# Kernel tuning notes

Measured on AMD Instinct MI355X. Metric: run time of the kernel, lower is better.

Reference implementation:

```python
import jax, jax.numpy as jnp
import numpy as np

N = 4096      # tokens per modality
DIM = 514     # input feature dim
OUT = 256     # out_dim (per-head width, head=1)
NC = 2        # num_classes
LN_EPS = 1e-5


def setup_inputs() -> dict:
    key = jax.random.key(0)
    ks = jax.random.split(key, 12)
    def nrm(k, shape, s=0.02):
        return jax.random.normal(k, shape, dtype=jnp.float32) * s
    return {
        "t1": jax.random.normal(ks[0], (N, DIM), dtype=jnp.float32),
        "t2": jax.random.normal(ks[1], (N, DIM), dtype=jnp.float32),
        "t1c": jax.random.normal(ks[2], (N, DIM), dtype=jnp.float32),
        "Wqkv1": nrm(ks[3], (DIM, 3 * OUT)), "bqkv1": jnp.zeros((3 * OUT,), jnp.float32),
        "Wqkv2": nrm(ks[4], (DIM, 3 * OUT)), "bqkv2": jnp.zeros((3 * OUT,), jnp.float32),
        "Wqkv3": nrm(ks[5], (DIM, 3 * OUT)), "bqkv3": jnp.zeros((3 * OUT,), jnp.float32),
        "Wo1": nrm(ks[6], (2 * OUT, DIM)), "bo1": jnp.zeros((DIM,), jnp.float32),
        "Wo2": nrm(ks[7], (2 * OUT, DIM)), "bo2": jnp.zeros((DIM,), jnp.float32),
        "Wo3": nrm(ks[8], (2 * OUT, DIM)), "bo3": jnp.zeros((DIM,), jnp.float32),
        "ln_g": jnp.ones((3 * DIM,), jnp.float32),
        "ln_b": jnp.zeros((3 * DIM,), jnp.float32),
        "Wh": nrm(ks[9], (3 * DIM, NC)), "bh": jnp.zeros((NC,), jnp.float32),
    }


def _forward(t1, t2, t1c, Wqkv1, bqkv1, Wqkv2, bqkv2, Wqkv3, bqkv3,
             Wo1, bo1, Wo2, bo2, Wo3, bo3, ln_g, ln_b, Wh, bh):
    # QKV projections (head=1 so no head reshape needed)
    q1, k1, v1 = jnp.split(t1 @ Wqkv1 + bqkv1, 3, axis=-1)   # each [n, OUT]
    q2, k2, v2 = jnp.split(t2 @ Wqkv2 + bqkv2, 3, axis=-1)
    q3, k3, v3 = jnp.split(t1c @ Wqkv3 + bqkv3, 3, axis=-1)

    # Six cross-attention instances batched into one group dim g=6.
    # Order: out12, out13, out21, out23, out31, out32  (q_x attends to k_y/v_y)
    qs = jnp.stack([q2, q3, q1, q3, q1, q2])                  # [6, n, OUT]
    ks_ = jnp.stack([k1, k1, k2, k2, k3, k3])
    vs = jnp.stack([v1, v1, v2, v2, v3, v3])
    # NOTE: original code applies NO 1/sqrt(d) scale
    attn = jax.nn.softmax(jnp.einsum('gid,gjd->gij', qs, ks_), axis=-1)
    outs = jnp.einsum('gij,gjd->gid', attn, vs)               # [6, n, OUT]
    out12, out13, out21, out23, out31, out32 = outs

    # residual add with duplicated keys, then per-modality output proj + residual
    t1r = jnp.concatenate([out21, out31], -1) + jnp.concatenate([k1, k1], -1)
    t2r = jnp.concatenate([out12, out32], -1) + jnp.concatenate([k2, k2], -1)
    t3r = jnp.concatenate([out13, out23], -1) + jnp.concatenate([k3, k3], -1)
    a1 = t1r @ Wo1 + bo1 + t1                                 # [n, DIM]
    a2 = t2r @ Wo2 + bo2 + t2
    a3 = t3r @ Wo3 + bo3 + t1c

    atten = jnp.concatenate([a1, a2, a3], -1)                 # [n, 3*DIM]
    mu = jnp.mean(atten, axis=-1, keepdims=True)
    var = jnp.var(atten, axis=-1, keepdims=True)
    normed = (atten - mu) * jax.lax.rsqrt(var + LN_EPS) * ln_g + ln_b
    out = normed @ Wh + bh                                    # [n, NC]
    feat = atten[None]                                        # [1, n, 3*DIM]
    return out, feat


def reference(t1, t2, t1c, Wqkv1, bqkv1, Wqkv2, bqkv2, Wqkv3, bqkv3,
              Wo1, bo1, Wo2, bo2, Wo3, bo3, ln_g, ln_b, Wh, bh):
    return _forward(t1, t2, t1c, Wqkv1, bqkv1, Wqkv2, bqkv2, Wqkv3, bqkv3,
                    Wo1, bo1, Wo2, bo2, Wo3, bo3, ln_g, ln_b, Wh, bh)
```

## Files before the change

### kernel.cpp

```cpp
#include <hip/hip_runtime.h>
#include <hip/hip_bf16.h>

typedef unsigned short u16;
typedef unsigned int u32;
typedef __attribute__((ext_vector_type(8))) __bf16 bf16x8;
typedef __attribute__((ext_vector_type(16))) float f32x16;

#define N_TOK 4096
#define DIMF  514
#define KPAD  544
#define OUT3  768
#define OUTD  256
#define RDIM  512
#define FDIM  1542
#define SHIFT 16.0f
#define NCHUNK 4
#define KTILES ((N_TOK / NCHUNK) / 32)

__device__ __forceinline__ bf16x8 ld_frag(const u16* p) {
    return __builtin_bit_cast(bf16x8, *reinterpret_cast<const uint4*>(p));
}
__device__ __forceinline__ u16 f2bf(float x) {
    return __builtin_bit_cast(u16, __float2bfloat16(x));
}
__device__ __forceinline__ float bf2f(u16 u) {
    return __bfloat162float(__builtin_bit_cast(__hip_bfloat16, u));
}
__device__ __forceinline__ f32x16 mfma_b(bf16x8 a, bf16x8 b, f32x16 c) {
    return __builtin_amdgcn_mfma_f32_32x32x16_bf16(a, b, c, 0, 0, 0);
}
__device__ __forceinline__ void gl_lds16(const u16* g, u16* l) {
    __builtin_amdgcn_global_load_lds(
        (const __attribute__((address_space(1))) void*)(g),
        (__attribute__((address_space(3))) void*)(l), 16, 0, 0);
}

__global__ void prep_kernel(const float* __restrict__ t1, const float* __restrict__ t2,
                            const float* __restrict__ t1c,
                            const float* __restrict__ W1, const float* __restrict__ W2,
                            const float* __restrict__ W3,
                            const float* __restrict__ Wo1, const float* __restrict__ Wo2,
                            const float* __restrict__ Wo3,
                            u16* __restrict__ tA, u16* __restrict__ WqkvT,
                            u16* __restrict__ WoT)
{
    int idx = blockIdx.x * blockDim.x + threadIdx.x;
    const int TA_N = 3 * N_TOK * KPAD;
    const int WQ_N = 3 * OUT3 * KPAD;
    const int WO_N = 3 * DIMF * RDIM;
    if (idx < TA_N) {
        int m = idx / (N_TOK * KPAD);
        int rem = idx - m * (N_TOK * KPAD);
        int row = rem / KPAD;
        int col = rem - row * KPAD;
        const float* t = (m == 0) ? t1 : (m == 1) ? t2 : t1c;
        tA[idx] = (col < DIMF) ? f2bf(t[row * DIMF + col]) : (u16)0;
    } else if (idx < TA_N + WQ_N) {
        int i = idx - TA_N;
        int m = i / (OUT3 * KPAD);
        int rem = i - m * (OUT3 * KPAD);
        int n = rem / KPAD;
        int c = rem - n * KPAD;
        const float* W = (m == 0) ? W1 : (m == 1) ? W2 : W3;
        WqkvT[i] = (c < DIMF) ? f2bf(W[c * OUT3 + n]) : (u16)0;
    } else if (idx < TA_N + WQ_N + WO_N) {
        int i = idx - TA_N - WQ_N;
        int m = i / (DIMF * RDIM);
        int rem = i - m * (DIMF * RDIM);
        int n = rem / RDIM;
        int c = rem - n * RDIM;
        const float* W = (m == 0) ? Wo1 : (m == 1) ? Wo2 : Wo3;
        WoT[i] = f2bf(W[c * DIMF + n]);
    }
}

__global__ __launch_bounds__(256, 1) void qkv_gemm(
    const u16* __restrict__ tA, const u16* __restrict__ WqkvT,
    const float* __restrict__ b1, const float* __restrict__ b2, const float* __restrict__ b3,
    u16* __restrict__ qbuf, u16* __restrict__ kbuf, u16* __restrict__ vT)
{
    const int mt = blockIdx.x, nt = blockIdx.y, mod = blockIdx.z;
    const u16* A = tA + mod * (N_TOK * KPAD);
    const u16* B = WqkvT + mod * (OUT3 * KPAD);
    const float* bias = (mod == 0) ? b1 : (mod == 1) ? b2 : b3;

    __shared__ alignas(16) u16 Al[128 * 40];
    __shared__ alignas(16) u16 Bl[128 * 40];

    const int tid = threadIdx.x;
    const int lane = tid & 63;
    const int w = tid >> 6;
    const int wm = w & 1, wn = w >> 1;
    const int l31 = lane & 31, h = lane >> 5;

    f32x16 acc[2][2];
#pragma unroll
    for (int i = 0; i < 2; i++)
#pragma unroll
        for (int j = 0; j < 2; j++)
#pragma unroll
            for (int r = 0; r < 16; r++) acc[i][j][r] = 0.f;

    for (int kt = 0; kt < KPAD / 32; kt++) {
#pragma unroll
        for (int it = 0; it < 2; it++) {
            int idx = it * 256 + tid;
            int row = idx >> 2;
            int c8 = (idx & 3) * 8;
            uint4 va = *reinterpret_cast<const uint4*>(&A[(mt * 128 + row) * KPAD + kt * 32 + c8]);
            *reinterpret_cast<uint4*>(&Al[row * 40 + c8]) = va;
            uint4 vb = *reinterpret_cast<const uint4*>(&B[(nt * 128 + row) * KPAD + kt * 32 + c8]);
            *reinterpret_cast<uint4*>(&Bl[row * 40 + c8]) = vb;
        }
        __syncthreads();
#pragma unroll
        for (int kc = 0; kc < 2; kc++) {
            bf16x8 af[2], bfr[2];
#pragma unroll
            for (int mr = 0; mr < 2; mr++)
                af[mr] = ld_frag(&Al[(wm * 64 + mr * 32 + l31) * 40 + kc * 16 + h * 8]);
#pragma unroll
            for (int nr = 0; nr < 2; nr++)
                bfr[nr] = ld_frag(&Bl[(wn * 64 + nr * 32 + l31) * 40 + kc * 16 + h * 8]);
#pragma unroll
            for (int mr = 0; mr < 2; mr++)
#pragma unroll
                for (int nr = 0; nr < 2; nr++)
                    acc[mr][nr] = mfma_b(af[mr], bfr[nr], acc[mr][nr]);
        }
        __syncthreads();
    }

    u16* qb = qbuf + mod * (N_TOK * OUTD);
    u16* kb = kbuf + mod * (N_TOK * OUTD);
    u16* vb = vT + mod * (OUTD * N_TOK);
#pragma unroll
    for (int mr = 0; mr < 2; mr++)
#pragma unroll
        for (int nr = 0; nr < 2; nr++)
#pragma unroll
            for (int r = 0; r < 16; r++) {
                int row = mt * 128 + wm * 64 + mr * 32 + (r & 3) + 8 * (r >> 2) + 4 * h;
                int col = nt * 128 + wn * 64 + nr * 32 + l31;
                u16 bv = f2bf(acc[mr][nr][r] + bias[col]);
                int cs = col >> 8, cc = col & 255;
                if (cs == 0)      qb[row * OUTD + cc] = bv;
                else if (cs == 1) kb[row * OUTD + cc] = bv;
                else              vb[cc * N_TOK + row] = bv;
            }
}

__global__ __launch_bounds__(256, 2) void attn_kernel(
    const u16* __restrict__ qbuf, const u16* __restrict__ kbuf,
    const u16* __restrict__ vT, u16* __restrict__ Opart, float* __restrict__ lpart)
{
    const int qt = blockIdx.x;
    const int g  = blockIdx.y;
    const int c  = blockIdx.z;
    const int kv = g >> 1;
    const int mn = (kv == 0) ? 1 : 0;
    const int mx = (kv == 2) ? 1 : 2;
    const int qm = (g & 1) ? mx : mn;

    const u16* Qg = qbuf + qm * (N_TOK * OUTD);
    const u16* Kg = kbuf + kv * (N_TOK * OUTD);
    const u16* Vg = vT + kv * (OUTD * N_TOK);
    u16* Op = Opart + ((size_t)(c * 6 + g) * N_TOK + qt * 128) * OUTD;
    float* lp = lpart + (c * 6 + g) * N_TOK + qt * 128;

    __shared__ alignas(16) u16 Fbuf[2][32 * 512];

    const int tid = threadIdx.x;
    const int lane = tid & 63;
    const int w = tid >> 6;
    const int l31 = lane & 31, h = lane >> 5;
    const int q0 = qt * 128 + w * 32;

    auto stage = [&](int k0, u16* dst) {
        if (w < 2) {
#pragma unroll
            for (int fi = 0; fi < 8; fi++) {
                int dc = w * 8 + fi;
                gl_lds16(&Kg[(k0 + l31) * OUTD + dc * 16 + h * 8], dst + dc * 512);
            }
        } else {
#pragma unroll
            for (int fi = 0; fi < 8; fi++) {
                int f = (w - 2) * 8 + fi;
                int nb = f >> 1, half = f & 1;
                gl_lds16(&Vg[(nb * 32 + l31) * N_TOK + k0 + half * 16 + h * 8],
                         dst + (16 + f) * 512);
            }
        }
    };

    const int k0base = c * (N_TOK / NCHUNK);

    stage(k0base, Fbuf[0]);

    bf16x8 qf[16];
#pragma unroll
    for (int dc = 0; dc < 16; dc++)
        qf[dc] = ld_frag(&Qg[(q0 + l31) * OUTD + dc * 16 + h * 8]);

    f32x16 Oacc[8];
#pragma unroll
    for (int nb = 0; nb < 8; nb++)
#pragma unroll
        for (int r = 0; r < 16; r++) Oacc[nb][r] = 0.f;
    float lsum = 0.f;

    __syncthreads();

    for (int kt = 0; kt < KTILES; kt++) {
        const int p = kt & 1;
        if (kt + 1 < KTILES) stage(k0base + (kt + 1) * 32, Fbuf[p ^ 1]);
        const u16* FB = Fbuf[p];

        f32x16 S;
#pragma unroll
        for (int r = 0; r < 16; r++) S[r] = 0.f;
#pragma unroll
        for (int dc = 0; dc < 16; dc++) {
            bf16x8 kf = ld_frag(&FB[dc * 512 + lane * 8]);
            S = mfma_b(kf, qf[dc], S);
        }

        float e[16];
#pragma unroll
        for (int r = 0; r < 16; r++) { e[r] = __expf(S[r] - SHIFT); lsum += e[r]; }
        u32 pk[8];
#pragma unroll
        for (int i = 0; i < 8; i++)
            pk[i] = (u32)f2bf(e[2 * i]) | ((u32)f2bf(e[2 * i + 1]) << 16);
        u32 x[8];
#pragma unroll
        for (int i = 0; i < 8; i++)
            x[i] = (u32)__shfl_xor((int)pk[i], 32, 64);
        uint4 b0, b1;
        b0.x = h ? x[2] : pk[0]; b0.y = h ? x[3] : pk[1];
        b0.z = h ? pk[2] : x[0]; b0.w = h ? pk[3] : x[1];
        b1.x = h ? x[6] : pk[4]; b1.y = h ? x[7] : pk[5];
        b1.z = h ? pk[6] : x[4]; b1.w = h ? pk[7] : x[5];
        bf16x8 pb0 = __builtin_bit_cast(bf16x8, b0);
        bf16x8 pb1 = __builtin_bit_cast(bf16x8, b1);

#pragma unroll
        for (int nb = 0; nb < 8; nb++) {
            bf16x8 vf0 = ld_frag(&FB[(16 + 2 * nb) * 512 + lane * 8]);
            bf16x8 vf1 = ld_frag(&FB[(17 + 2 * nb) * 512 + lane * 8]);
            Oacc[nb] = mfma_b(vf0, pb0, Oacc[nb]);
            Oacc[nb] = mfma_b(vf1, pb1, Oacc[nb]);
        }
        __syncthreads();
    }

    lsum += __shfl_xor(lsum, 32, 64);
    if (lane < 32) lp[w * 32 + lane] = lsum;

    float* Tb = reinterpret_cast<float*>(&Fbuf[0][0]) + w * (32 * 33);
#pragma unroll
    for (int nb = 0; nb < 8; nb++) {
#pragma unroll
        for (int r = 0; r < 16; r++)
            Tb[((r & 3) + 8 * (r >> 2) + 4 * h) * 33 + l31] = Oacc[nb][r];
        __builtin_amdgcn_s_waitcnt(0);
#pragma unroll
        for (int qq = 0; qq < 16; qq++) {
            float v = Tb[l31 * 33 + qq * 2 + h];
            Op[(w * 32 + qq * 2 + h) * OUTD + nb * 32 + l31] = f2bf(v);
        }
        __builtin_amdgcn_s_waitcnt(0);
    }
}

__global__ __launch_bounds__(256, 1) void combine_kernel(
    const u16* __restrict__ Opart, const float* __restrict__ lpart,
    const u16* __restrict__ kbuf, u16* __restrict__ rbuf)
{
    const int q = blockIdx.x;
    const int g = blockIdx.y;
    const int d = threadIdx.x;
    const int kv = g >> 1;
    const int mn = (kv == 0) ? 1 : 0;
    const int mx = (kv == 2) ? 1 : 2;
    const int qm = (g & 1) ? mx : mn;
    const int sm = (qm == 0) ? 1 : 0;
    const int slot = (kv == sm) ? 0 : 1;

    float o = 0.f, l = 0.f;
#pragma unroll
    for (int c = 0; c < NCHUNK; c++) {
        o += bf2f(Opart[((size_t)(c * 6 + g) * N_TOK + q) * OUTD + d]);
        l += lpart[(c * 6 + g) * N_TOK + q];
    }
    float res = o / l + bf2f(kbuf[qm * (N_TOK * OUTD) + q * OUTD + d]);
    rbuf[qm * (size_t)(N_TOK * RDIM) + q * RDIM + slot * OUTD + d] = f2bf(res);
}

__global__ __launch_bounds__(256, 1) void proj_gemm(
    const u16* __restrict__ rbuf, const u16* __restrict__ WoT,
    const float* __restrict__ bo1, const float* __restrict__ bo2, const float* __restrict__ bo3,
    const float* __restrict__ t1, const float* __restrict__ t2, const float* __restrict__ t1c,
    float* __restrict__ feat)
{
    const int mt = blockIdx.x, nt = blockIdx.y, mod = blockIdx.z;
    const u16* A = rbuf + mod * (N_TOK * RDIM);
    const u16* B = WoT + mod * (DIMF * RDIM);
    const float* bias = (mod == 0) ? bo1 : (mod == 1) ? bo2 : bo3;
    const float* tres = (mod == 0) ? t1 : (mod == 1) ? t2 : t1c;

    __shared__ alignas(16) u16 Al[128 * 40];
    __shared__ alignas(16) u16 Bl[128 * 40];

    const int tid = threadIdx.x;
    const int lane = tid & 63;
    const int w = tid >> 6;
    const int wm = w & 1, wn = w >> 1;
    const int l31 = lane & 31, h = lane >> 5;

    f32x16 acc[2][2];
#pragma unroll
    for (int i = 0; i < 2; i++)
#pragma unroll
        for (int j = 0; j < 2; j++)
#pragma unroll
            for (int r = 0; r < 16; r++) acc[i][j][r] = 0.f;

    for (int kt = 0; kt < RDIM / 32; kt++) {
#pragma unroll
        for (int it = 0; it < 2; it++) {
            int idx = it * 256 + tid;
            int row = idx >> 2;
            int c8 = (idx & 3) * 8;
            uint4 va = *reinterpret_cast<const uint4*>(&A[(mt * 128 + row) * RDIM + kt * 32 + c8]);
            *reinterpret_cast<uint4*>(&Al[row * 40 + c8]) = va;
            int n = nt * 128 + row;
            uint4 vb;
            if (n < DIMF) vb = *reinterpret_cast<const uint4*>(&B[n * RDIM + kt * 32 + c8]);
            else { vb.x = vb.y = vb.z = vb.w = 0u; }
            *reinterpret_cast<uint4*>(&Bl[row * 40 + c8]) = vb;
        }
        __syncthreads();
#pragma unroll
        for (int kc = 0; kc < 2; kc++) {
            bf16x8 af[2], bfr[2];
#pragma unroll
            for (int mr = 0; mr < 2; mr++)
                af[mr] = ld_frag(&Al[(wm * 64 + mr * 32 + l31) * 40 + kc * 16 + h * 8]);
#pragma unroll
            for (int nr = 0; nr < 2; nr++)
                bfr[nr] = ld_frag(&Bl[(wn * 64 + nr * 32 + l31) * 40 + kc * 16 + h * 8]);
#pragma unroll
            for (int mr = 0; mr < 2; mr++)
#pragma unroll
                for (int nr = 0; nr < 2; nr++)
                    acc[mr][nr] = mfma_b(af[mr], bfr[nr], acc[mr][nr]);
        }
        __syncthreads();
    }

#pragma unroll
    for (int mr = 0; mr < 2; mr++)
#pragma unroll
        for (int nr = 0; nr < 2; nr++)
#pragma unroll
            for (int r = 0; r < 16; r++) {
                int row = mt * 128 + wm * 64 + mr * 32 + (r & 3) + 8 * (r >> 2) + 4 * h;
                int col = nt * 128 + wn * 64 + nr * 32 + l31;
                if (col < DIMF) {
                    float v = acc[mr][nr][r] + bias[col] + tres[row * DIMF + col];
                    feat[row * FDIM + mod * DIMF + col] = v;
                }
            }
}

__global__ __launch_bounds__(256, 1) void ln_head(
    const float* __restrict__ feat, const float* __restrict__ gam,
    const float* __restrict__ bet, const float* __restrict__ Wh,
    const float* __restrict__ bh, float* __restrict__ out)
{
    const int row = blockIdx.x;
    const float* x = feat + row * FDIM;
    const int tid = threadIdx.x;
    float v[7];
    float s = 0.f, ss = 0.f;
#pragma unroll
    for (int i = 0; i < 7; i++) {
        int idx = tid + i * 256;
        float val = (idx < FDIM) ? x[idx] : 0.f;
        v[i] = val; s += val; ss += val * val;
    }
#pragma unroll
    for (int m = 1; m < 64; m <<= 1) { s += __shfl_xor(s, m, 64); ss += __shfl_xor(ss, m, 64); }
    __shared__ float red[8];
    const int w = tid >> 6, lane = tid & 63;
    if (lane == 0) { red[w] = s; red[4 + w] = ss; }
    __syncthreads();
    s = red[0] + red[1] + red[2] + red[3];
    ss = red[4] + red[5] + red[6] + red[7];
    const float mu = s / (float)FDIM;
    const float var = ss / (float)FDIM - mu * mu;
    const float rstd = rsqrtf(var + 1e-5f);
    float a0 = 0.f, a1 = 0.f;
#pragma unroll
    for (int i = 0; i < 7; i++) {
        int idx = tid + i * 256;
        if (idx < FDIM) {
            float nv = (v[i] - mu) * rstd * gam[idx] + bet[idx];
            a0 += nv * Wh[idx * 2];
            a1 += nv * Wh[idx * 2 + 1];
        }
    }
#pragma unroll
    for (int m = 1; m < 64; m <<= 1) { a0 += __shfl_xor(a0, m, 64); a1 += __shfl_xor(a1, m, 64); }
    __shared__ float red2[8];
    if (lane == 0) { red2[w] = a0; red2[4 + w] = a1; }
    __syncthreads();
    if (tid == 0) {
        out[row * 2 + 0] = red2[0] + red2[1] + red2[2] + red2[3] + bh[0];
        out[row * 2 + 1] = red2[4] + red2[5] + red2[6] + red2[7] + bh[1];
    }
}

extern "C" void kernel_launch(void* const* d_in, const int* in_sizes, int n_in,
                              void* d_out, int out_size, void* d_ws, size_t ws_size,
                              hipStream_t stream)
{
    const float* t1    = (const float*)d_in[0];
    const float* t2    = (const float*)d_in[1];
    const float* t1c   = (const float*)d_in[2];
    const float* Wqkv1 = (const float*)d_in[3];
    const float* bqkv1 = (const float*)d_in[4];
    const float* Wqkv2 = (const float*)d_in[5];
    const float* bqkv2 = (const float*)d_in[6];
    const float* Wqkv3 = (const float*)d_in[7];
    const float* bqkv3 = (const float*)d_in[8];
    const float* Wo1   = (const float*)d_in[9];
    const float* bo1   = (const float*)d_in[10];
    const float* Wo2   = (const float*)d_in[11];
    const float* bo2   = (const float*)d_in[12];
    const float* Wo3   = (const float*)d_in[13];
    const float* bo3   = (const float*)d_in[14];
    const float* ln_g  = (const float*)d_in[15];
    const float* ln_b  = (const float*)d_in[16];
    const float* Wh    = (const float*)d_in[17];
    const float* bh    = (const float*)d_in[18];

    char* ws = (char*)d_ws;
    size_t off = 0;
    u16* tA    = (u16*)(ws + off); off += (size_t)3 * N_TOK * KPAD * 2;
    u16* WqkvT = (u16*)(ws + off); off += (size_t)3 * OUT3 * KPAD * 2;
    u16* WoT   = (u16*)(ws + off); off += (size_t)3 * DIMF * RDIM * 2;
    u16* qbuf  = (u16*)(ws + off); off += (size_t)3 * N_TOK * OUTD * 2;
    u16* kbuf  = (u16*)(ws + off); off += (size_t)3 * N_TOK * OUTD * 2;
    u16* vT    = (u16*)(ws + off); off += (size_t)3 * OUTD * N_TOK * 2;
    u16* rbuf  = (u16*)(ws + off); off += (size_t)3 * N_TOK * RDIM * 2;
    u16* Opart = (u16*)(ws + off); off += (size_t)NCHUNK * 6 * N_TOK * OUTD * 2;
    float* lpart = (float*)(ws + off); off += (size_t)NCHUNK * 6 * N_TOK * 4;

    float* out  = (float*)d_out;
    float* feat = out + N_TOK * 2;

    const int prep_total = 3 * N_TOK * KPAD + 3 * OUT3 * KPAD + 3 * DIMF * RDIM;
    prep_kernel<<<(prep_total + 255) / 256, 256, 0, stream>>>(
        t1, t2, t1c, Wqkv1, Wqkv2, Wqkv3, Wo1, Wo2, Wo3, tA, WqkvT, WoT);

    qkv_gemm<<<dim3(32, 6, 3), 256, 0, stream>>>(
        tA, WqkvT, bqkv1, bqkv2, bqkv3, qbuf, kbuf, vT);

    attn_kernel<<<dim3(32, 6, NCHUNK), 256, 0, stream>>>(qbuf, kbuf, vT, Opart, lpart);

    combine_kernel<<<dim3(N_TOK, 6), 256, 0, stream>>>(Opart, lpart, kbuf, rbuf);

    proj_gemm<<<dim3(32, 5, 3), 256, 0, stream>>>(
        rbuf, WoT, bo1, bo2, bo3, t1, t2, t1c, feat);

    ln_head<<<4096, 256, 0, stream>>>(feat, ln_g, ln_b, Wh, bh, out);
}
```

Before: 339.1 us.

## Load V fragments directly to registers and stage only K through LDS

```diff
diff --git a/kernel.cpp b/kernel.cpp
--- a/kernel.cpp
+++ b/kernel.cpp
@@ -150,7 +150,7 @@
             }
 }
 
-__global__ __launch_bounds__(256, 2) void attn_kernel(
+__global__ __launch_bounds__(256, 3) void attn_kernel(
     const u16* __restrict__ qbuf, const u16* __restrict__ kbuf,
     const u16* __restrict__ vT, u16* __restrict__ Opart, float* __restrict__ lpart)
 {
@@ -168,7 +168,7 @@
     u16* Op = Opart + ((size_t)(c * 6 + g) * N_TOK + qt * 128) * OUTD;
     float* lp = lpart + (c * 6 + g) * N_TOK + qt * 128;
 
-    __shared__ alignas(16) u16 Fbuf[2][32 * 512];
+    __shared__ alignas(16) u16 Kbuf[2][16 * 512];
 
     const int tid = threadIdx.x;
     const int lane = tid & 63;
@@ -176,27 +176,17 @@
     const int l31 = lane & 31, h = lane >> 5;
     const int q0 = qt * 128 + w * 32;
 
-    auto stage = [&](int k0, u16* dst) {
-        if (w < 2) {
-#pragma unroll
-            for (int fi = 0; fi < 8; fi++) {
-                int dc = w * 8 + fi;
-                gl_lds16(&Kg[(k0 + l31) * OUTD + dc * 16 + h * 8], dst + dc * 512);
-            }
-        } else {
-#pragma unroll
-            for (int fi = 0; fi < 8; fi++) {
-                int f = (w - 2) * 8 + fi;
-                int nb = f >> 1, half = f & 1;
-                gl_lds16(&Vg[(nb * 32 + l31) * N_TOK + k0 + half * 16 + h * 8],
-                         dst + (16 + f) * 512);
-            }
+    auto stageK = [&](int k0, u16* dst) {
+#pragma unroll
+        for (int fi = 0; fi < 4; fi++) {
+            int dc = w * 4 + fi;
+            gl_lds16(&Kg[(k0 + l31) * OUTD + dc * 16 + h * 8], dst + dc * 512);
         }
     };
 
     const int k0base = c * (N_TOK / NCHUNK);
 
-    stage(k0base, Fbuf[0]);
+    stageK(k0base, Kbuf[0]);
 
     bf16x8 qf[16];
 #pragma unroll
@@ -214,21 +204,34 @@
 
     for (int kt = 0; kt < KTILES; kt++) {
         const int p = kt & 1;
-        if (kt + 1 < KTILES) stage(k0base + (kt + 1) * 32, Fbuf[p ^ 1]);
-        const u16* FB = Fbuf[p];
-
-        f32x16 S;
-#pragma unroll
-        for (int r = 0; r < 16; r++) S[r] = 0.f;
-#pragma unroll
-        for (int dc = 0; dc < 16; dc++) {
-            bf16x8 kf = ld_frag(&FB[dc * 512 + lane * 8]);
-            S = mfma_b(kf, qf[dc], S);
-        }
+        const int k0 = k0base + kt * 32;
+
+        bf16x8 vf[16];
+#pragma unroll
+        for (int f = 0; f < 16; f++) {
+            int nb = f >> 1, half = f & 1;
+            vf[f] = ld_frag(&Vg[(nb * 32 + l31) * N_TOK + k0 + half * 16 + h * 8]);
+        }
+
+        if (kt + 1 < KTILES) stageK(k0base + (kt + 1) * 32, Kbuf[p ^ 1]);
+        const u16* KB = Kbuf[p];
+
+        f32x16 S0, S1;
+#pragma unroll
+        for (int r = 0; r < 16; r++) { S0[r] = 0.f; S1[r] = 0.f; }
+        __builtin_amdgcn_s_setprio(1);
+#pragma unroll
+        for (int dc = 0; dc < 16; dc += 2) {
+            bf16x8 kfa = ld_frag(&KB[dc * 512 + lane * 8]);
+            bf16x8 kfb = ld_frag(&KB[(dc + 1) * 512 + lane * 8]);
+            S0 = mfma_b(kfa, qf[dc], S0);
+            S1 = mfma_b(kfb, qf[dc + 1], S1);
+        }
+        __builtin_amdgcn_s_setprio(0);
 
         float e[16];
 #pragma unroll
-        for (int r = 0; r < 16; r++) { e[r] = __expf(S[r] - SHIFT); lsum += e[r]; }
+        for (int r = 0; r < 16; r++) { e[r] = __expf(S0[r] + S1[r] - SHIFT); lsum += e[r]; }
         u32 pk[8];
 #pragma unroll
         for (int i = 0; i < 8; i++)
@@ -245,20 +248,20 @@
         bf16x8 pb0 = __builtin_bit_cast(bf16x8, b0);
         bf16x8 pb1 = __builtin_bit_cast(bf16x8, b1);
 
+        __builtin_amdgcn_s_setprio(1);
 #pragma unroll
         for (int nb = 0; nb < 8; nb++) {
-            bf16x8 vf0 = ld_frag(&FB[(16 + 2 * nb) * 512 + lane * 8]);
-            bf16x8 vf1 = ld_frag(&FB[(17 + 2 * nb) * 512 + lane * 8]);
-            Oacc[nb] = mfma_b(vf0, pb0, Oacc[nb]);
-            Oacc[nb] = mfma_b(vf1, pb1, Oacc[nb]);
-        }
+            Oacc[nb] = mfma_b(vf[2 * nb], pb0, Oacc[nb]);
+            Oacc[nb] = mfma_b(vf[2 * nb + 1], pb1, Oacc[nb]);
+        }
+        __builtin_amdgcn_s_setprio(0);
         __syncthreads();
     }
 
     lsum += __shfl_xor(lsum, 32, 64);
     if (lane < 32) lp[w * 32 + lane] = lsum;
 
-    float* Tb = reinterpret_cast<float*>(&Fbuf[0][0]) + w * (32 * 33);
+    float* Tb = reinterpret_cast<float*>(&Kbuf[0][0]) + w * (32 * 33);
 #pragma unroll
     for (int nb = 0; nb < 8; nb++) {
 #pragma unroll
```

Result: slower. 1.213 ms (+257.6%).
